# Performance work log

Hardware: AMD Instinct MI355X
Metric: run time of the kernel (lower is better)

## Reference

```python
import jax, jax.numpy as jnp
import numpy as np

D, FF, R, B, S, H, HD = 1024, 4096, 16, 8, 512, 16, 64
EPS = 1e-5


def _lora(x, w, b, la, lb):
    # base linear (w is [out,in] torch-style) + low-rank LoRA add
    return x @ w.T + b + (x @ la) @ lb


def _ln(x, w, b):
    mu = jnp.mean(x, axis=-1, keepdims=True)
    var = jnp.mean((x - mu) ** 2, axis=-1, keepdims=True)
    return (x - mu) * jax.lax.rsqrt(var + EPS) * w + b


def setup_inputs() -> dict:
    key = jax.random.key(0)
    ks = jax.random.split(key, 32)
    i = iter(range(32))
    nrm = lambda shape, scale=0.02: jax.random.normal(ks[next(i)], shape, jnp.float32) * scale
    inp = {
        'x': jax.random.normal(ks[next(i)], (B, S, D), jnp.float32),
        'attention_mask': jnp.zeros((B, 1, 1, S), jnp.float32),
        'w_q': nrm((D, D)), 'b_q': nrm((D,)), 'la_q': nrm((D, R)), 'lb_q': nrm((R, D)),
        'w_k': nrm((D, D)), 'b_k': nrm((D,)), 'la_k': nrm((D, R)), 'lb_k': nrm((R, D)),
        'w_v': nrm((D, D)), 'b_v': nrm((D,)), 'la_v': nrm((D, R)), 'lb_v': nrm((R, D)),
        'w_o': nrm((D, D)), 'b_o': nrm((D,)), 'la_o': nrm((D, R)), 'lb_o': nrm((R, D)),
        'nw1': jnp.ones((D,), jnp.float32), 'nb1': jnp.zeros((D,), jnp.float32),
        'w_up': nrm((FF, D)), 'b_up': nrm((FF,)), 'la_up': nrm((D, R)), 'lb_up': nrm((R, FF)),
        'w_down': nrm((D, FF)), 'b_down': nrm((D,)), 'la_down': nrm((FF, R)), 'lb_down': nrm((R, D)),
        'nw2': jnp.ones((D,), jnp.float32), 'nb2': jnp.zeros((D,), jnp.float32),
        'num_heads': H, 'head_dim': HD,
    }
    return inp


def reference(x, attention_mask, w_q, b_q, la_q, lb_q, w_k, b_k, la_k, lb_k,
              w_v, b_v, la_v, lb_v, w_o, b_o, la_o, lb_o, nw1, nb1,
              w_up, b_up, la_up, lb_up, w_down, b_down, la_down, lb_down,
              nw2, nb2, num_heads, head_dim):
    bsz, q_len, d = x.shape
    to_heads = lambda t: t.reshape(bsz, q_len, num_heads, head_dim).transpose(0, 2, 1, 3)
    q = to_heads(_lora(x, w_q, b_q, la_q, lb_q))  # [B,H,S,HD]
    k = to_heads(_lora(x, w_k, b_k, la_k, lb_k))
    v = to_heads(_lora(x, w_v, b_v, la_v, lb_v))
    s = jnp.einsum('bhqd,bhkd->bhqk', q, k) / np.sqrt(head_dim) + attention_mask
    a = jax.nn.softmax(s, axis=-1)
    o = jnp.einsum('bhqk,bhkd->bhqd', a, v).transpose(0, 2, 1, 3).reshape(bsz, q_len, d)
    o_final = _lora(o, w_o, b_o, la_o, lb_o) + x
    x_medium = _ln(o_final, nw1, nb1)
    up = _lora(x_medium, w_up, b_up, la_up, lb_up)
    fn = jax.nn.gelu(up, approximate=False)  # torch F.gelu default = exact erf
    down = _lora(fn, w_down, b_down, la_down, lb_down) + x_medium
    return _ln(down, nw2, nb2)
```

## Files before the change

kernel.cpp:

```cpp
#include <hip/hip_runtime.h>
#include <math.h>

typedef unsigned short u16;
typedef __attribute__((ext_vector_type(8))) short short8;
typedef __attribute__((ext_vector_type(4))) float floatx4;

#define DEV __device__ __forceinline__

DEV u16 f2bs(float f){ union{float f; unsigned u;} v; v.f=f; unsigned r = v.u + 0x7fffu + ((v.u>>16)&1u); return (u16)(r>>16); }
DEV float bs2f(u16 u){ union{float f; unsigned u;} v; v.u = ((unsigned)u)<<16; return v.f; }

DEV float gelu_f(float x){
  float u2 = 2.f * x * (0.7978845608028654f + 0.03567740813636141f*x*x);
  float e = __expf(u2);
  float th = 1.f - 2.f/(e + 1.f);
  return 0.5f*x*(1.f + th);
}

#define GLL16(G,L) __builtin_amdgcn_global_load_lds((__attribute__((address_space(1))) const void*)(G), (__attribute__((address_space(3))) void*)(L), 16, 0, 0)
#define SB0() __builtin_amdgcn_sched_barrier(0)

enum { EP_BF16=0, EP_F32RES=3, EP_GELU=4 };

DEV void swizzle_bid(int orig, int gx, int gy, int& bx, int& by){
  const int nwg = gx*gy;
  const int q = nwg >> 3, r = nwg & 7;
  const int xcd = orig & 7, idx = orig >> 3;
  const int logical = (xcd < r) ? xcd*(q+1) + idx : r*(q+1) + (xcd-r)*q + idx;
  const int G = 8;
  const int per = G*gx;
  const int gid = logical / per;
  const int rem = logical - gid*per;
  const int by0 = gid*G;
  const int rows = min(G, gy - by0);
  by = by0 + rem % rows;
  bx = rem / rows;
}

template<int MODE,bool LORA,bool SWZ>
__global__ __launch_bounds__(512,2) void gemm8(
    const u16* __restrict__ A, int lda,
    const u16* __restrict__ B, int ldb,
    int K,
    u16* __restrict__ obf, float* __restrict__ of32, int ldc,
    const float* __restrict__ bias,
    const u16* __restrict__ tA, int tlda,
    const u16* __restrict__ lbB,
    const float* __restrict__ resid)
{
  __shared__ u16 sm8[65536];
  const int tid = threadIdx.x;
  const int lane = tid & 63, wave = tid >> 6;
  const int wr = wave >> 2, wc = wave & 3;
  const int row16 = lane & 15, kgrp = lane >> 4;
  int bx = blockIdx.x, by = blockIdx.y;
  if constexpr (SWZ)
    swizzle_bid(blockIdx.y*gridDim.x + blockIdx.x, gridDim.x, gridDim.y, bx, by);
  const int bm0 = by*256, bn0 = bx*256;
  const u16* Ab = A + (long)bm0*lda;
  const u16* Bb = B + (long)bn0*ldb;
  const int tsel = (LORA && tlda==192) ? ((bn0>>10)*64) : 0;
  const int srow = lane >> 3;
  const int gcol = ((lane&7) ^ srow) * 8;
  const int nKT = K >> 6;
  const int nIT = nKT + (LORA ? 1 : 0);

  auto stage_half = [&](int kt, int h, int buf){
    const int isB = h & 1, hi = h >> 1;
    const u16* src; long ld;
    if (!LORA || kt < nKT){
      if (isB){ src = Bb + kt*64; ld = ldb; } else { src = Ab + kt*64; ld = lda; }
    } else {
      if (isB){ src = lbB + (long)bn0*64; ld = 64; }
      else    { src = tA + (long)bm0*tlda + tsel; ld = tlda; }
    }
    char* base = (char*)sm8 + buf*65536 + isB*32768 + hi*16384;
    #pragma unroll
    for (int rr=0; rr<2; ++rr){
      int g = wave + rr*8;
      GLL16(src + (long)(hi*128 + g*8 + srow)*ld + gcol, base + g*1024);
    }
  };
  auto ldA = [&](int buf, int mh, int i, int ks)->short8{
    int r_ = mh*128 + wr*64 + i*16 + row16;
    return *(const short8*)((const char*)sm8 + buf*65536 + r_*128 + (((ks*4+kgrp) ^ (r_&7))<<4));
  };
  auto ldB = [&](int buf, int nh, int j, int ks)->short8{
    int r_ = nh*128 + wc*32 + j*16 + row16;
    return *(const short8*)((const char*)sm8 + buf*65536 + 32768 + r_*128 + (((ks*4+kgrp) ^ (r_&7))<<4));
  };

  floatx4 acc[8][4];
  #pragma unroll
  for (int i=0;i<8;i++)
    #pragma unroll
    for (int j=0;j<4;j++)
      acc[i][j] = (floatx4){0.f,0.f,0.f,0.f};

  stage_half(0,0,0); stage_half(0,1,0); stage_half(0,2,0); stage_half(0,3,0);
  if (nIT>1){ stage_half(1,0,1); stage_half(1,1,1); }

#define MM8(mh,nh,AR,BR) \
  { _Pragma("unroll") \
    for (int i=0;i<4;i++) \
      _Pragma("unroll") \
      for (int j=0;j<2;j++) \
        _Pragma("unroll") \
        for (int ks=0;ks<2;ks++) \
          acc[(mh)*4+i][(nh)*2+j] = __builtin_amdgcn_mfma_f32_16x16x32_bf16(AR[i][ks], BR[j][ks], acc[(mh)*4+i][(nh)*2+j], 0, 0, 0); }

  int buf = 0;
  for (int t=0; t<nIT; ++t, buf^=1){
    const bool n1 = (t+1 < nIT), n2 = (t+2 < nIT);
    if (n1){ stage_half(t+1,2,buf^1); stage_half(t+1,3,buf^1); }
    if (n1) asm volatile("s_waitcnt vmcnt(8)" ::: "memory");
    else    asm volatile("s_waitcnt vmcnt(0)" ::: "memory");
    __builtin_amdgcn_s_barrier();

    short8 a0[4][2], a1[4][2], b0[2][2], b1[2][2];
    #pragma unroll
    for (int i=0;i<4;i++){ a0[i][0]=ldA(buf,0,i,0); a0[i][1]=ldA(buf,0,i,1); }
    #pragma unroll
    for (int j=0;j<2;j++){ b0[j][0]=ldB(buf,0,j,0); b0[j][1]=ldB(buf,0,j,1); }
    SB0();
    #pragma unroll
    for (int j=0;j<2;j++){ b1[j][0]=ldB(buf,1,j,0); b1[j][1]=ldB(buf,1,j,1); }
    asm volatile("s_waitcnt lgkmcnt(4)" ::: "memory");
    SB0();
    __builtin_amdgcn_s_setprio(1);
    MM8(0,0,a0,b0);
    __builtin_amdgcn_s_setprio(0);
    SB0();
    #pragma unroll
    for (int i=0;i<4;i++){ a1[i][0]=ldA(buf,1,i,0); a1[i][1]=ldA(buf,1,i,1); }
    asm volatile("s_waitcnt lgkmcnt(8)" ::: "memory");
    SB0();
    __builtin_amdgcn_s_setprio(1);
    MM8(0,1,a0,b1);
    __builtin_amdgcn_s_setprio(0);
    asm volatile("s_waitcnt lgkmcnt(0)" ::: "memory");
    SB0();
    __builtin_amdgcn_s_barrier();
    if (n2){ stage_half(t+2,0,buf); stage_half(t+2,1,buf); }
    __builtin_amdgcn_s_setprio(1);
    MM8(1,1,a1,b1);
    MM8(1,0,a1,b0);
    __builtin_amdgcn_s_setprio(0);
  }
#undef MM8

  #pragma unroll
  for (int mi=0;mi<8;mi++){
    const int mloc = (mi<4) ? (wr*64 + mi*16) : (128 + wr*64 + (mi-4)*16);
    #pragma unroll
    for (int r=0;r<4;r++){
      const long mg = bm0 + mloc + kgrp*4 + r;
      #pragma unroll
      for (int ni=0;ni<4;ni++){
        const int nloc = (ni<2) ? (wc*32 + ni*16) : (128 + wc*32 + (ni-2)*16);
        const int ng = bn0 + nloc + row16;
        float v = acc[mi][ni][r] + bias[ng];
        if constexpr (MODE==EP_F32RES){
          v += resid[mg*ldc + ng];
          of32[mg*ldc + ng] = v;
        } else if constexpr (MODE==EP_GELU){
          obf[mg*ldc + ng] = f2bs(gelu_f(v));
        } else {
          obf[mg*ldc + ng] = f2bs(v);
        }
      }
    }
  }
}

template<int BM,int BN,int WM,int WN,int MODE,bool LORA,bool SWZ>
__global__ __launch_bounds__((BM/WM)*(BN/WN)*64) void gemm_bt(
    const u16* __restrict__ A, int lda,
    const u16* __restrict__ B, int ldb,
    int K,
    u16* __restrict__ obf, float* __restrict__ of32, int ldc,
    const float* __restrict__ bias,
    const u16* __restrict__ tA, int tlda,
    const u16* __restrict__ lbB,
    const float* __restrict__ resid)
{
  constexpr int NWM = BM/WM, NWN = BN/WN, NW = NWM*NWN;
  constexpr int FM = WM/16, FN = WN/16;
  constexpr int TILE = (BM+BN)*64;
  constexpr int LPT = (BM+BN)/(8*NW);
  static_assert(NW==4 || NW==8, "4 or 8 waves");
  static_assert((BM/8)%NW==0 && (BN/8)%NW==0, "row-group striping");
  __shared__ u16 ab[2*TILE];

  const int tid = threadIdx.x;
  const int lane = tid & 63, wave = tid >> 6;
  const int wr = wave / NWN, wc = wave % NWN;
  const int row16 = lane & 15, kgrp = lane >> 4;
  int bx = blockIdx.x, by = blockIdx.y;
  if constexpr (SWZ)
    swizzle_bid(blockIdx.y*gridDim.x + blockIdx.x, gridDim.x, gridDim.y, bx, by);
  const int bm0 = by * BM, bn0 = bx * BN;

  const u16* Ab = A + (long)bm0*lda;
  const u16* Bb = B + (long)bn0*ldb;
  const int tsel = (LORA && tlda==192) ? ((bn0>>10)*64) : 0;
  const int srow = lane >> 3;
  const int gcol = ((lane&7) ^ srow) * 8;

  const int nKT = K >> 6;
  const int nIT = nKT + (LORA ? 1 : 0);

  auto stage = [&](int kt, int buf){
    const u16 *Ak, *Bk; long la_, lb_;
    if (!LORA || kt < nKT){ Ak = Ab + kt*64; la_ = lda; Bk = Bb + kt*64; lb_ = ldb; }
    else { Ak = tA + (long)bm0*tlda + tsel; la_ = tlda; Bk = lbB + (long)bn0*64; lb_ = 64; }
    char* l = (char*)(ab + buf*TILE);
    #pragma unroll
    for (int g0=0; g0<BM/8; g0+=NW){
      int g = g0 + wave;
      GLL16(Ak + (long)(g*8 + srow)*la_ + gcol, l + g*1024);
    }
    #pragma unroll
    for (int g0=0; g0<BN/8; g0+=NW){
      int g = g0 + wave;
      GLL16(Bk + (long)(g*8 + srow)*lb_ + gcol, l + BM*128 + g*1024);
    }
  };

  floatx4 acc[FM][FN];
  #pragma unroll
  for (int i=0;i<FM;i++)
    #pragma unroll
    for (int j=0;j<FN;j++)
      acc[i][j] = (floatx4){0.f,0.f,0.f,0.f};

  stage(0, 0);
  if (nIT > 1) stage(1, 1);
  int cur = 0;
  for (int kt=0; kt<nIT; ++kt){
    if (kt+1 < nIT) asm volatile("s_waitcnt vmcnt(%0)" :: "n"(LPT) : "memory");
    else            asm volatile("s_waitcnt vmcnt(0)" ::: "memory");
    __builtin_amdgcn_s_barrier();

    const char* lds = (const char*)(ab + cur*TILE);
    __builtin_amdgcn_s_setprio(1);
    #pragma unroll
    for (int ks=0; ks<2; ++ks){
      short8 af[FM], bfr[FN];
      #pragma unroll
      for (int mi=0;mi<FM;mi++){
        int r_ = wr*WM + mi*16 + row16;
        af[mi] = *(const short8*)(lds + r_*128 + (((ks*4 + kgrp) ^ (r_&7))<<4));
      }
      #pragma unroll
      for (int ni=0;ni<FN;ni++){
        int r_ = wc*WN + ni*16 + row16;
        bfr[ni] = *(const short8*)(lds + BM*128 + r_*128 + (((ks*4 + kgrp) ^ (r_&7))<<4));
      }
      #pragma unroll
      for (int mi=0;mi<FM;mi++)
        #pragma unroll
        for (int ni=0;ni<FN;ni++)
          acc[mi][ni] = __builtin_amdgcn_mfma_f32_16x16x32_bf16(af[mi], bfr[ni], acc[mi][ni], 0, 0, 0);
    }
    __builtin_amdgcn_s_setprio(0);

    asm volatile("s_waitcnt lgkmcnt(0)" ::: "memory");
    __builtin_amdgcn_sched_barrier(0);
    __builtin_amdgcn_s_barrier();
    if (kt+2 < nIT) stage(kt+2, cur);
    cur ^= 1;
  }

  #pragma unroll
  for (int mi=0;mi<FM;mi++){
    #pragma unroll
    for (int r=0;r<4;r++){
      const int ml = wr*WM + mi*16 + kgrp*4 + r;
      const long mg = bm0 + ml;
      #pragma unroll
      for (int ni=0;ni<FN;ni++){
        const int nl = wc*WN + ni*16 + row16;
        const int ng = bn0 + nl;
        float v = acc[mi][ni][r] + bias[ng];
        if constexpr (MODE==EP_F32RES){
          v += resid[mg*ldc + ng];
          of32[mg*ldc + ng] = v;
        } else if constexpr (MODE==EP_GELU){
          obf[mg*ldc + ng] = f2bs(gelu_f(v));
        } else {
          obf[mg*ldc + ng] = f2bs(v);
        }
      }
    }
  }
}

template<int NT>
__global__ __launch_bounds__(64) void lora_mfma(
    const u16* __restrict__ A, const int K,
    const u16* __restrict__ lat,
    u16* __restrict__ t, int tld)
{
  const int lane = threadIdx.x & 63;
  const int c = lane & 15, kg = lane >> 4;
  const int m0 = blockIdx.x * 16;
  const u16* Arow = A + (long)(m0 + c)*K + kg*8;
  const u16* Brow = lat + (long)c*K + kg*8;
  floatx4 acc[NT];
  #pragma unroll
  for (int tj=0;tj<NT;tj++) acc[tj] = (floatx4){0.f,0.f,0.f,0.f};
  const int nKS = K >> 5;
  #pragma unroll 4
  for (int ks=0; ks<nKS; ++ks){
    short8 a = *(const short8*)(Arow + ks*32);
    #pragma unroll
    for (int tj=0; tj<NT; ++tj){
      short8 b = *(const short8*)(Brow + (long)tj*16*K + ks*32);
      acc[tj] = __builtin_amdgcn_mfma_f32_16x16x32_bf16(a, b, acc[tj], 0, 0, 0);
    }
  }
  #pragma unroll
  for (int tj=0; tj<NT; ++tj)
    #pragma unroll
    for (int r=0;r<4;r++){
      u16* dst = t + (long)(m0 + kg*4 + r)*tld + tj*64;
      dst[c] = f2bs(acc[tj][r]);
      dst[16+c] = 0; dst[32+c] = 0; dst[48+c] = 0;
    }
}

__global__ __launch_bounds__(256) void flash_attn(
    const u16* __restrict__ qkv,
    const u16* __restrict__ vt,
    const float* __restrict__ mask,
    u16* __restrict__ attn_o)
{
  __shared__ u16 sm[33792];
  u16* Qs = sm;
  u16* Ps = sm + 24576;

  const int tid = threadIdx.x, lane = tid & 63, wave = tid >> 6;
  const int c = lane & 15, kg = lane >> 4;
  const int qt = blockIdx.x;
  const int z  = blockIdx.y;
  const int b = z >> 4, h = z & 15;
  const int q0 = qt * 128;
  const int srow = lane >> 3;
  const int scol = ((lane&7) ^ srow) * 8;

  const u16* kbase = qkv + ((long)(b*512))*3072 + 1024 + h*64;
  const u16* vbase = vt + (long)z*64*512;

  auto stage_kv = [&](int kv, int buf){
    char* Kd = (char*)(sm + 8192  + buf*4096);
    char* Vd = (char*)(sm + 16384 + buf*4096);
    #pragma unroll
    for (int i=0;i<2;i++){
      int rb = i*32 + wave*8;
      GLL16(kbase + (long)(kv*64 + rb + srow)*3072 + scol, Kd + rb*128);
      GLL16(vbase + (long)(rb + srow)*512 + kv*64 + scol, Vd + rb*128);
    }
  };

  {
    const u16* src = qkv + ((long)(b*512 + q0))*3072 + h*64;
    #pragma unroll
    for (int i=0;i<4;i++){
      int rb = i*32 + wave*8;
      GLL16(src + (long)(rb + srow)*3072 + scol, (char*)Qs + rb*128);
    }
  }
  stage_kv(0, 0);
  __syncthreads();

  auto ld_swz = [&](const u16* t, int row, int koff8) -> short8 {
    return *(const short8*)((const char*)t + row*128 + ((koff8 ^ (row&7))<<4));
  };

  short8 af[2][2];
  #pragma unroll
  for (int mi=0;mi<2;mi++)
    #pragma unroll
    for (int ks=0;ks<2;ks++)
      af[mi][ks] = ld_swz(Qs, wave*32 + mi*16 + c, ks*4 + kg);

  floatx4 o_acc[2][4];
  float m_run[2][4], l_run[2][4];
  #pragma unroll
  for (int mi=0;mi<2;mi++){
    #pragma unroll
    for (int dj=0;dj<4;dj++) o_acc[mi][dj] = (floatx4){0.f,0.f,0.f,0.f};
    #pragma unroll
    for (int r=0;r<4;r++){ m_run[mi][r] = -3.0e38f; l_run[mi][r] = 0.f; }
  }

  int cur = 0;
  for (int kv=0; kv<8; ++kv){
    if (kv+1 < 8) stage_kv(kv+1, cur^1);
    const u16* Ks = sm + 8192  + cur*4096;
    const u16* Vs = sm + 16384 + cur*4096;

    floatx4 s_acc[2][4];
    #pragma unroll
    for (int mi=0;mi<2;mi++)
      #pragma unroll
      for (int ni=0;ni<4;ni++)
        s_acc[mi][ni] = (floatx4){0.f,0.f,0.f,0.f};
    #pragma unroll
    for (int ks=0;ks<2;ks++){
      short8 bf[4];
      #pragma unroll
      for (int ni=0;ni<4;ni++)
        bf[ni] = ld_swz(Ks, ni*16 + c, ks*4 + kg);
      #pragma unroll
      for (int mi=0;mi<2;mi++)
        #pragma unroll
        for (int ni=0;ni<4;ni++)
          s_acc[mi][ni] = __builtin_amdgcn_mfma_f32_16x16x32_bf16(af[mi][ks], bf[ni], s_acc[mi][ni], 0, 0, 0);
    }

    float mv[4];
    #pragma unroll
    for (int ni=0;ni<4;ni++) mv[ni] = mask[b*512 + kv*64 + ni*16 + c];

    #pragma unroll
    for (int mi=0;mi<2;mi++){
      #pragma unroll
      for (int r=0;r<4;r++){
        float s0 = s_acc[mi][0][r]*0.125f + mv[0];
        float s1 = s_acc[mi][1][r]*0.125f + mv[1];
        float s2 = s_acc[mi][2][r]*0.125f + mv[2];
        float s3 = s_acc[mi][3][r]*0.125f + mv[3];
        float tmax = fmaxf(fmaxf(s0,s1), fmaxf(s2,s3));
        #pragma unroll
        for (int o=1;o<16;o<<=1) tmax = fmaxf(tmax, __shfl_xor(tmax, o));
        const float mnew = fmaxf(m_run[mi][r], tmax);
        const float p0 = __expf(s0 - mnew), p1 = __expf(s1 - mnew);
        const float p2 = __expf(s2 - mnew), p3 = __expf(s3 - mnew);
        float psum = p0+p1+p2+p3;
        #pragma unroll
        for (int o=1;o<16;o<<=1) psum += __shfl_xor(psum, o);
        const float alpha = __expf(m_run[mi][r] - mnew);
        l_run[mi][r] = l_run[mi][r]*alpha + psum;
        m_run[mi][r] = mnew;
        #pragma unroll
        for (int dj=0;dj<4;dj++) o_acc[mi][dj][r] *= alpha;
        const int rl = mi*16 + kg*4 + r;
        u16* pw = Ps + wave*2304 + rl*72;
        pw[c]      = f2bs(p0);
        pw[16 + c] = f2bs(p1);
        pw[32 + c] = f2bs(p2);
        pw[48 + c] = f2bs(p3);
      }
    }
    __syncthreads();

    #pragma unroll
    for (int ks=0;ks<2;ks++){
      short8 pa[2], vb[4];
      #pragma unroll
      for (int mi=0;mi<2;mi++)
        pa[mi] = *(const short8*)&Ps[wave*2304 + (mi*16 + c)*72 + ks*32 + kg*8];
      #pragma unroll
      for (int dj=0;dj<4;dj++)
        vb[dj] = ld_swz(Vs, dj*16 + c, ks*4 + kg);
      __builtin_amdgcn_s_setprio(1);
      #pragma unroll
      for (int mi=0;mi<2;mi++)
        #pragma unroll
        for (int dj=0;dj<4;dj++)
          o_acc[mi][dj] = __builtin_amdgcn_mfma_f32_16x16x32_bf16(pa[mi], vb[dj], o_acc[mi][dj], 0, 0, 0);
      __builtin_amdgcn_s_setprio(0);
    }
    __syncthreads();
    cur ^= 1;
  }

  #pragma unroll
  for (int mi=0;mi<2;mi++){
    #pragma unroll
    for (int r=0;r<4;r++){
      const float inv = 1.f / l_run[mi][r];
      const int s_g = q0 + wave*32 + mi*16 + kg*4 + r;
      u16* dst = attn_o + (long)(b*512 + s_g)*1024 + h*64;
      #pragma unroll
      for (int dj=0;dj<4;dj++)
        dst[dj*16 + c] = f2bs(o_acc[mi][dj][r]*inv);
    }
  }
}

__global__ __launch_bounds__(256) void convert_bulk(
  const float* __restrict__ x,
  const float* __restrict__ wq, const float* __restrict__ wk, const float* __restrict__ wv,
  const float* __restrict__ wo, const float* __restrict__ wup, const float* __restrict__ wdn,
  u16* __restrict__ xb, u16* __restrict__ wqkv, u16* __restrict__ wob,
  u16* __restrict__ wupb, u16* __restrict__ wdnb)
{
  const long NX = 4194304, NWt = 1048576;
  const long T4 = (NX + 3*NWt + NWt + NX + NX) >> 2;
  for (long i4 = (long)blockIdx.x*256 + threadIdx.x; i4 < T4; i4 += (long)gridDim.x*256){
    long j = i4 << 2;
    const float* src; u16* dst; long soff, doff;
    if (j < NX){ src=x; dst=xb; soff=j; doff=j; }
    else { j -= NX;
      if (j < 3*NWt){ int p=(int)(j>>20); src = p==0?wq:(p==1?wk:wv); dst=wqkv; soff = j & (NWt-1); doff = j; }
      else { j -= 3*NWt;
        if (j < NWt){ src=wo; dst=wob; soff=j; doff=j; }
        else { j -= NWt;
          if (j < NX){ src=wup; dst=wupb; soff=j; doff=j; }
          else { j -= NX; src=wdn; dst=wdnb; soff=j; doff=j; }
        }
      }
    }
    const float4 v = *(const float4*)(src + soff);
    ushort4 o;
    o.x = f2bs(v.x); o.y = f2bs(v.y); o.z = f2bs(v.z); o.w = f2bs(v.w);
    *(ushort4*)(dst + doff) = o;
  }
}

__global__ __launch_bounds__(256) void convert_small(
  const float* __restrict__ bq, const float* __restrict__ bk, const float* __restrict__ bv,
  const float* __restrict__ lbq, const float* __restrict__ lbk, const float* __restrict__ lbv,
  const float* __restrict__ lbo, const float* __restrict__ lbup, const float* __restrict__ lbdn,
  const float* __restrict__ laq, const float* __restrict__ lak, const float* __restrict__ lav,
  const float* __restrict__ lao, const float* __restrict__ laup, const float* __restrict__ ladn,
  float* __restrict__ biascat, u16* __restrict__ lbtqkv, u16* __restrict__ lbto,
  u16* __restrict__ lbtup, u16* __restrict__ lbtdn,
  u16* __restrict__ latqkv, u16* __restrict__ lato,
  u16* __restrict__ latup, u16* __restrict__ latdn)
{
  long i = (long)blockIdx.x*256 + threadIdx.x;
  if (i < 3072){ int p=(int)(i>>10); biascat[i] = (p==0?bq:(p==1?bk:bv))[i&1023]; return; }
  i -= 3072;
  if (i < 49152){ int k=(int)(i/3072), n=(int)(i%3072); int p=n>>10;
    const float* l = p==0?lbq:(p==1?lbk:lbv);
    u16* d = lbtqkv + (long)n*64 + k;
    d[0] = f2bs(l[k*1024 + (n&1023)]); d[16]=0; d[32]=0; d[48]=0; return; }
  i -= 49152;
  if (i < 16384){ int k=(int)(i>>10), n=(int)(i&1023);
    u16* d = lbto + (long)n*64 + k;
    d[0] = f2bs(lbo[k*1024+n]); d[16]=0; d[32]=0; d[48]=0; return; }
  i -= 16384;
  if (i < 65536){ int k=(int)(i>>12), n=(int)(i&4095);
    u16* d = lbtup + (long)n*64 + k;
    d[0] = f2bs(lbup[k*4096+n]); d[16]=0; d[32]=0; d[48]=0; return; }
  i -= 65536;
  if (i < 16384){ int k=(int)(i>>10), n=(int)(i&1023);
    u16* d = lbtdn + (long)n*64 + k;
    d[0] = f2bs(lbdn[k*1024+n]); d[16]=0; d[32]=0; d[48]=0; return; }
  i -= 16384;
  if (i < 49152){ int r=(int)(i>>10), k=(int)(i&1023);
    const float* l = r<16 ? laq : (r<32 ? lak : lav);
    latqkv[i] = f2bs(l[k*16 + (r&15)]); return; }
  i -= 49152;
  if (i < 16384){ int r=(int)(i>>10), k=(int)(i&1023);
    lato[i] = f2bs(lao[k*16+r]); return; }
  i -= 16384;
  if (i < 16384){ int r=(int)(i>>10), k=(int)(i&1023);
    latup[i] = f2bs(laup[k*16+r]); return; }
  i -= 16384;
  if (i < 65536){ int r=(int)(i>>12), k=(int)(i&4095);
    latdn[i] = f2bs(ladn[k*16+r]); }
}

__global__ __launch_bounds__(256) void transpose_v(const u16* __restrict__ qkv, u16* __restrict__ vt){
  const int st = blockIdx.x;
  const int z = blockIdx.y;
  const int b = z >> 4, h = z & 15;
  __shared__ u16 tile[64][68];
  const int t = threadIdx.x;
  const int q16 = t & 15, g16 = t >> 4;
  const u16* src = qkv + ((long)(b*512 + st*64))*3072 + 2048 + h*64;
  #pragma unroll
  for (int i=0;i<4;i++){
    int s_l = i*16 + g16;
    const u16* pp = src + (long)s_l*3072 + q16*4;
    #pragma unroll
    for (int jj=0;jj<4;jj++) tile[s_l][q16*4+jj] = pp[jj];
  }
  __syncthreads();
  u16* dst = vt + (long)z*64*512 + st*64;
  #pragma unroll
  for (int i=0;i<4;i++){
    int d_l = i*16 + g16;
    int s_l = q16*4;
    unsigned long long v = (unsigned long long)tile[s_l][d_l]
      | ((unsigned long long)tile[s_l+1][d_l] << 16)
      | ((unsigned long long)tile[s_l+2][d_l] << 32)
      | ((unsigned long long)tile[s_l+3][d_l] << 48);
    *(unsigned long long*)(dst + (long)d_l*512 + s_l) = v;
  }
}

__global__ __launch_bounds__(256) void ln_k(
    const float* __restrict__ in, float* __restrict__ outf, u16* __restrict__ outb,
    const float* __restrict__ gam, const float* __restrict__ bet)
{
  const long row = blockIdx.x;
  const float4 v = ((const float4*)(in + row*1024))[threadIdx.x];
  float s = v.x+v.y+v.z+v.w;
  float q = v.x*v.x + v.y*v.y + v.z*v.z + v.w*v.w;
  const int lane = threadIdx.x & 63, w = threadIdx.x >> 6;
  __shared__ float rs[4], rq[4];
  #pragma unroll
  for (int o=32;o;o>>=1){ s += __shfl_down(s,o); q += __shfl_down(q,o); }
  if (!lane){ rs[w]=s; rq[w]=q; }
  __syncthreads();
  const float S = rs[0]+rs[1]+rs[2]+rs[3];
  const float Q = rq[0]+rq[1]+rq[2]+rq[3];
  const float mu = S*(1.f/1024.f);
  const float var = Q*(1.f/1024.f) - mu*mu;
  const float rstd = rsqrtf(var + 1e-5f);
  const float4 g = ((const float4*)gam)[threadIdx.x];
  const float4 b = ((const float4*)bet)[threadIdx.x];
  float4 o;
  o.x = (v.x-mu)*rstd*g.x + b.x;
  o.y = (v.y-mu)*rstd*g.y + b.y;
  o.z = (v.z-mu)*rstd*g.z + b.z;
  o.w = (v.w-mu)*rstd*g.w + b.w;
  if (outf) ((float4*)(outf + row*1024))[threadIdx.x] = o;
  if (outb){
    uint2 u;
    u.x = (unsigned)f2bs(o.x) | ((unsigned)f2bs(o.y) << 16);
    u.y = (unsigned)f2bs(o.z) | ((unsigned)f2bs(o.w) << 16);
    ((uint2*)(outb + row*1024))[threadIdx.x] = u;
  }
}

extern "C" void kernel_launch(void* const* d_in, const int* in_sizes, int n_in,
                              void* d_out, int out_size, void* d_ws, size_t ws_size,
                              hipStream_t stream) {
  const float* x      = (const float*)d_in[0];
  const float* mask   = (const float*)d_in[1];
  const float* w_q    = (const float*)d_in[2];
  const float* b_q    = (const float*)d_in[3];
  const float* la_q   = (const float*)d_in[4];
  const float* lb_q   = (const float*)d_in[5];
  const float* w_k    = (const float*)d_in[6];
  const float* b_k    = (const float*)d_in[7];
  const float* la_k   = (const float*)d_in[8];
  const float* lb_k   = (const float*)d_in[9];
  const float* w_v    = (const float*)d_in[10];
  const float* b_v    = (const float*)d_in[11];
  const float* la_v   = (const float*)d_in[12];
  const float* lb_v   = (const float*)d_in[13];
  const float* w_o    = (const float*)d_in[14];
  const float* b_o    = (const float*)d_in[15];
  const float* la_o   = (const float*)d_in[16];
  const float* lb_o   = (const float*)d_in[17];
  const float* nw1    = (const float*)d_in[18];
  const float* nb1    = (const float*)d_in[19];
  const float* w_up   = (const float*)d_in[20];
  const float* b_up   = (const float*)d_in[21];
  const float* la_up  = (const float*)d_in[22];
  const float* lb_up  = (const float*)d_in[23];
  const float* w_dn   = (const float*)d_in[24];
  const float* b_dn   = (const float*)d_in[25];
  const float* la_dn  = (const float*)d_in[26];
  const float* lb_dn  = (const float*)d_in[27];
  const float* nw2    = (const float*)d_in[28];
  const float* nb2    = (const float*)d_in[29];
  float* out = (float*)d_out;

  char* ws = (char*)d_ws;
  size_t used = 0;
  auto alloc = [&](size_t bytes) -> char* {
    char* p = ws + used;
    used += (bytes + 255) & ~(size_t)255;
    return p;
  };
  u16*   xb      = (u16*)  alloc(4194304*2);
  u16*   wqkv    = (u16*)  alloc(3145728*2);
  u16*   wob     = (u16*)  alloc(1048576*2);
  u16*   wupb    = (u16*)  alloc(4194304*2);
  u16*   wdnb    = (u16*)  alloc(4194304*2);
  float* biascat = (float*)alloc(3072*4);
  u16*   lbtqkv  = (u16*)  alloc((size_t)3072*64*2);
  u16*   lbto    = (u16*)  alloc((size_t)1024*64*2);
  u16*   lbtup   = (u16*)  alloc((size_t)4096*64*2);
  u16*   lbtdn   = (u16*)  alloc((size_t)1024*64*2);
  u16*   latqkv  = (u16*)  alloc(48*1024*2);
  u16*   lato    = (u16*)  alloc(16*1024*2);
  u16*   latup   = (u16*)  alloc(16*1024*2);
  u16*   latdn   = (u16*)  alloc(16*4096*2);
  u16*   t_all   = (u16*)  alloc((size_t)4096*192*2);
  u16*   t_o     = (u16*)  alloc((size_t)4096*64*2);
  u16*   t_up    = (u16*)  alloc((size_t)4096*64*2);
  u16*   t_dn    = (u16*)  alloc((size_t)4096*64*2);
  u16*   qkv     = (u16*)  alloc((size_t)4096*3072*2);
  u16*   vt      = (u16*)  alloc((size_t)128*64*512*2);
  u16*   attn_o  = (u16*)  alloc(4194304*2);
  float* o_final = (float*)alloc((size_t)4194304*4);
  float* x_med   = (float*)alloc((size_t)4194304*4);
  u16*   x_med_b = (u16*)  alloc(4194304*2);
  u16*   fn      = (u16*)  alloc((size_t)4096*4096*2);
  if (used > ws_size) return;

  convert_bulk<<<2048, 256, 0, stream>>>(x, w_q, w_k, w_v, w_o, w_up, w_dn,
                                         xb, wqkv, wob, wupb, wdnb);
  convert_small<<<1164, 256, 0, stream>>>(b_q, b_k, b_v, lb_q, lb_k, lb_v,
                                          lb_o, lb_up, lb_dn,
                                          la_q, la_k, la_v, la_o, la_up, la_dn,
                                          biascat, lbtqkv, lbto, lbtup, lbtdn,
                                          latqkv, lato, latup, latdn);
  lora_mfma<3><<<256, 64, 0, stream>>>(xb, 1024, latqkv, t_all, 192);
  gemm8<EP_BF16,true,true><<<dim3(12,16,1), 512, 0, stream>>>(
      xb, 1024, wqkv, 1024, 1024, qkv, nullptr, 3072,
      biascat, t_all, 192, lbtqkv, nullptr);
  transpose_v<<<dim3(8,128), 256, 0, stream>>>(qkv, vt);
  flash_attn<<<dim3(4,128), 256, 0, stream>>>(qkv, vt, mask, attn_o);
  lora_mfma<1><<<256, 64, 0, stream>>>(attn_o, 1024, lato, t_o, 64);
  gemm_bt<64,128,32,64,EP_F32RES,true,true><<<dim3(8,64,1), 256, 0, stream>>>(
      attn_o, 1024, wob, 1024, 1024, nullptr, o_final, 1024,
      b_o, t_o, 64, lbto, x);
  ln_k<<<4096, 256, 0, stream>>>(o_final, x_med, x_med_b, nw1, nb1);
  lora_mfma<1><<<256, 64, 0, stream>>>(x_med_b, 1024, latup, t_up, 64);
  gemm8<EP_GELU,true,true><<<dim3(16,16,1), 512, 0, stream>>>(
      x_med_b, 1024, wupb, 1024, 1024, fn, nullptr, 4096,
      b_up, t_up, 64, lbtup, nullptr);
  lora_mfma<1><<<256, 64, 0, stream>>>(fn, 4096, latdn, t_dn, 64);
  gemm_bt<64,128,32,64,EP_F32RES,true,true><<<dim3(8,64,1), 256, 0, stream>>>(
      fn, 4096, wdnb, 4096, 4096, nullptr, out, 1024,
      b_dn, t_dn, 64, lbtdn, x_med);
  ln_k<<<4096, 256, 0, stream>>>(out, out, nullptr, nw2, nb2);
}
```

Before: 274.7 us.

## Split-K the down-projection GEMM and its LoRA kernel, reduce in LayerNorm

The down-projection GEMM (K=4096) now runs as two K halves along grid z. Half 0 adds bias, residual and the LoRA term. Half 1 writes raw partial sums to a new fp32 buffer, and the final LayerNorm adds the two partials before normalising. The LoRA-down kernel also splits K across two waves and combines them through shared memory. This doubles the block count for a grid that only had 512 blocks, in exchange for an extra 16MB fp32 write and read of partials.

```diff
diff --git a/kernel.cpp b/kernel.cpp
--- a/kernel.cpp
+++ b/kernel.cpp
@@ -173,7 +173,7 @@
   }
 }
 
-template<int BM,int BN,int WM,int WN,int MODE,bool LORA,bool SWZ>
+template<int BM,int BN,int WM,int WN,int MODE,bool LORA,bool SWZ,bool SPLITK>
 __global__ __launch_bounds__((BM/WM)*(BN/WN)*64) void gemm_bt(
     const u16* __restrict__ A, int lda,
     const u16* __restrict__ B, int ldb,
@@ -182,7 +182,8 @@
     const float* __restrict__ bias,
     const u16* __restrict__ tA, int tlda,
     const u16* __restrict__ lbB,
-    const float* __restrict__ resid)
+    const float* __restrict__ resid,
+    float* __restrict__ of32b)
 {
   constexpr int NWM = BM/WM, NWN = BN/WN, NW = NWM*NWN;
   constexpr int FM = WM/16, FN = WN/16;
@@ -200,19 +201,24 @@
   if constexpr (SWZ)
     swizzle_bid(blockIdx.y*gridDim.x + blockIdx.x, gridDim.x, gridDim.y, bx, by);
   const int bm0 = by * BM, bn0 = bx * BN;
-
-  const u16* Ab = A + (long)bm0*lda;
-  const u16* Bb = B + (long)bn0*ldb;
+  int kz = 0;
+  if constexpr (SPLITK) kz = blockIdx.z;
+  const int Keff = SPLITK ? (K >> 1) : K;
+  const long koff = SPLITK ? (long)kz * Keff : 0;
+
+  const u16* Ab = A + (long)bm0*lda + koff;
+  const u16* Bb = B + (long)bn0*ldb + koff;
   const int tsel = (LORA && tlda==192) ? ((bn0>>10)*64) : 0;
   const int srow = lane >> 3;
   const int gcol = ((lane&7) ^ srow) * 8;
 
-  const int nKT = K >> 6;
-  const int nIT = nKT + (LORA ? 1 : 0);
+  const int nKT = Keff >> 6;
+  const bool doLora = LORA && (!SPLITK || kz == 0);
+  const int nIT = nKT + (doLora ? 1 : 0);
 
   auto stage = [&](int kt, int buf){
     const u16 *Ak, *Bk; long la_, lb_;
-    if (!LORA || kt < nKT){ Ak = Ab + kt*64; la_ = lda; Bk = Bb + kt*64; lb_ = ldb; }
+    if (kt < nKT){ Ak = Ab + kt*64; la_ = lda; Bk = Bb + kt*64; lb_ = ldb; }
     else { Ak = tA + (long)bm0*tlda + tsel; la_ = tlda; Bk = lbB + (long)bn0*64; lb_ = 64; }
     char* l = (char*)(ab + buf*TILE);
     #pragma unroll
@@ -282,6 +288,10 @@
       for (int ni=0;ni<FN;ni++){
         const int nl = wc*WN + ni*16 + row16;
         const int ng = bn0 + nl;
+        if (SPLITK && kz == 1){
+          of32b[mg*ldc + ng] = acc[mi][ni][r];
+          continue;
+        }
         float v = acc[mi][ni][r] + bias[ng];
         if constexpr (MODE==EP_F32RES){
           v += resid[mg*ldc + ng];
@@ -296,21 +306,22 @@
   }
 }
 
-template<int NT>
-__global__ __launch_bounds__(64) void lora_mfma(
+template<int NT,int KS>
+__global__ __launch_bounds__(64*KS) void lora_mfma(
     const u16* __restrict__ A, const int K,
     const u16* __restrict__ lat,
     u16* __restrict__ t, int tld)
 {
-  const int lane = threadIdx.x & 63;
+  const int lane = threadIdx.x & 63, wv = threadIdx.x >> 6;
   const int c = lane & 15, kg = lane >> 4;
   const int m0 = blockIdx.x * 16;
-  const u16* Arow = A + (long)(m0 + c)*K + kg*8;
-  const u16* Brow = lat + (long)c*K + kg*8;
+  const int Kw = K / KS;
+  const u16* Arow = A + (long)(m0 + c)*K + (long)wv*Kw + kg*8;
+  const u16* Brow = lat + (long)c*K + (long)wv*Kw + kg*8;
   floatx4 acc[NT];
   #pragma unroll
   for (int tj=0;tj<NT;tj++) acc[tj] = (floatx4){0.f,0.f,0.f,0.f};
-  const int nKS = K >> 5;
+  const int nKS = Kw >> 5;
   #pragma unroll 4
   for (int ks=0; ks<nKS; ++ks){
     short8 a = *(const short8*)(Arow + ks*32);
@@ -319,6 +330,21 @@
       short8 b = *(const short8*)(Brow + (long)tj*16*K + ks*32);
       acc[tj] = __builtin_amdgcn_mfma_f32_16x16x32_bf16(a, b, acc[tj], 0, 0, 0);
     }
+  }
+  if constexpr (KS == 2){
+    __shared__ float red[NT*256];
+    if (wv == 1){
+      #pragma unroll
+      for (int tj=0;tj<NT;tj++)
+        #pragma unroll
+        for (int r=0;r<4;r++) red[(tj*4+r)*64 + lane] = acc[tj][r];
+    }
+    __syncthreads();
+    if (wv == 1) return;
+    #pragma unroll
+    for (int tj=0;tj<NT;tj++)
+      #pragma unroll
+      for (int r=0;r<4;r++) acc[tj][r] += red[(tj*4+r)*64 + lane];
   }
   #pragma unroll
   for (int tj=0; tj<NT; ++tj)
@@ -596,11 +622,16 @@
 }
 
 __global__ __launch_bounds__(256) void ln_k(
-    const float* __restrict__ in, float* __restrict__ outf, u16* __restrict__ outb,
+    const float* __restrict__ in, const float* __restrict__ in2,
+    float* __restrict__ outf, u16* __restrict__ outb,
     const float* __restrict__ gam, const float* __restrict__ bet)
 {
   const long row = blockIdx.x;
-  const float4 v = ((const float4*)(in + row*1024))[threadIdx.x];
+  float4 v = ((const float4*)(in + row*1024))[threadIdx.x];
+  if (in2){
+    const float4 v2 = ((const float4*)(in2 + row*1024))[threadIdx.x];
+    v.x += v2.x; v.y += v2.y; v.z += v2.z; v.w += v2.w;
+  }
   float s = v.x+v.y+v.z+v.w;
   float q = v.x*v.x + v.y*v.y + v.z*v.z + v.w*v.w;
   const int lane = threadIdx.x & 63, w = threadIdx.x >> 6;
@@ -697,6 +728,7 @@
   float* x_med   = (float*)alloc((size_t)4194304*4);
   u16*   x_med_b = (u16*)  alloc(4194304*2);
   u16*   fn      = (u16*)  alloc((size_t)4096*4096*2);
+  float* p_dn    = (float*)alloc((size_t)4194304*4);
   if (used > ws_size) return;
 
   convert_bulk<<<2048, 256, 0, stream>>>(x, w_q, w_k, w_v, w_o, w_up, w_dn,
@@ -706,24 +738,24 @@
                                           la_q, la_k, la_v, la_o, la_up, la_dn,
                                           biascat, lbtqkv, lbto, lbtup, lbtdn,
                                           latqkv, lato, latup, latdn);
-  lora_mfma<3><<<256, 64, 0, stream>>>(xb, 1024, latqkv, t_all, 192);
+  lora_mfma<3,1><<<256, 64, 0, stream>>>(xb, 1024, latqkv, t_all, 192);
   gemm8<EP_BF16,true,true><<<dim3(12,16,1), 512, 0, stream>>>(
       xb, 1024, wqkv, 1024, 1024, qkv, nullptr, 3072,
       biascat, t_all, 192, lbtqkv, nullptr);
   transpose_v<<<dim3(8,128), 256, 0, stream>>>(qkv, vt);
   flash_attn<<<dim3(4,128), 256, 0, stream>>>(qkv, vt, mask, attn_o);
-  lora_mfma<1><<<256, 64, 0, stream>>>(attn_o, 1024, lato, t_o, 64);
-  gemm_bt<64,128,32,64,EP_F32RES,true,true><<<dim3(8,64,1), 256, 0, stream>>>(
+  lora_mfma<1,1><<<256, 64, 0, stream>>>(attn_o, 1024, lato, t_o, 64);
+  gemm_bt<64,128,32,64,EP_F32RES,true,true,false><<<dim3(8,64,1), 256, 0, stream>>>(
       attn_o, 1024, wob, 1024, 1024, nullptr, o_final, 1024,
-      b_o, t_o, 64, lbto, x);
-  ln_k<<<4096, 256, 0, stream>>>(o_final, x_med, x_med_b, nw1, nb1);
-  lora_mfma<1><<<256, 64, 0, stream>>>(x_med_b, 1024, latup, t_up, 64);
+      b_o, t_o, 64, lbto, x, nullptr);
+  ln_k<<<4096, 256, 0, stream>>>(o_final, nullptr, x_med, x_med_b, nw1, nb1);
+  lora_mfma<1,1><<<256, 64, 0, stream>>>(x_med_b, 1024, latup, t_up, 64);
   gemm8<EP_GELU,true,true><<<dim3(16,16,1), 512, 0, stream>>>(
       x_med_b, 1024, wupb, 1024, 1024, fn, nullptr, 4096,
       b_up, t_up, 64, lbtup, nullptr);
-  lora_mfma<1><<<256, 64, 0, stream>>>(fn, 4096, latdn, t_dn, 64);
-  gemm_bt<64,128,32,64,EP_F32RES,true,true><<<dim3(8,64,1), 256, 0, stream>>>(
-      fn, 4096, wdnb, 4096, 4096, nullptr, out, 1024,
-      b_dn, t_dn, 64, lbtdn, x_med);
-  ln_k<<<4096, 256, 0, stream>>>(out, out, nullptr, nw2, nb2);
-}
+  lora_mfma<1,2><<<256, 128, 0, stream>>>(fn, 4096, latdn, t_dn, 64);
+  gemm_bt<64,128,32,64,EP_F32RES,true,true,true><<<dim3(8,64,2), 256, 0, stream>>>(
+      fn, 4096, wdnb, 4096, 4096, nullptr, o_final, 1024,
+      b_dn, t_dn, 64, lbtdn, x_med, p_dn);
+  ln_k<<<4096, 256, 0, stream>>>(o_final, p_dn, out, nullptr, nw2, nb2);
+}
```

New measurement: 270.6 us. No clear change (-1.5%).
